# Kernel optimization log

Hardware: AMD Instinct MI355X
Metric: run time of the kernel (lower is better)

## Reference

```python
import jax, jax.numpy as jnp
import numpy as np

LN_EPS = 1e-5


def _mlp(x, W1, b1, W2, b2, g, beta):
    # build_mlp_d: Linear -> ReLU -> Linear -> LayerNorm (mlp_layers=2, lay_norm=True)
    h = jax.nn.relu(x @ W1 + b1)
    h = h @ W2 + b2
    mu = jnp.mean(h, axis=-1, keepdims=True)
    var = jnp.var(h, axis=-1, keepdims=True)
    return (h - mu) * jax.lax.rsqrt(var + LN_EPS) * g + beta


def setup_inputs() -> dict:
    E, N, L, EIF = 524288, 65536, 128, 3
    key = jax.random.key(0)
    ks = iter(jax.random.split(key, 48))
    def rn(shape, s=1.0):
        return jax.random.normal(next(ks), shape, dtype=jnp.float32) * s
    inp = {}
    inp["edge_index"] = jax.random.randint(next(ks), (2, E), 0, N)
    inp["edge_dx_"] = rn((E, 3))
    inp["edge_attr"] = rn((E, EIF))
    for nm in ["vector_a", "vector_b", "vector_c",
               "senders_v_t_", "senders_v_tm1_", "senders_w_t_", "senders_w_tm1_",
               "senders_a_t_", "senders_alpha_t_",
               "receivers_v_t_", "receivers_v_tm1_", "receivers_w_t_", "receivers_w_tm1_",
               "receivers_a_t_", "receivers_alpha_t_"]:
        inp[nm] = rn((E, 3))
    inp["node_latent"] = rn((N, L))
    def mlp_params(pfx, din):
        inp[pfx + "_W1"] = rn((din, L), 0.05)
        inp[pfx + "_b1"] = jnp.zeros((L,), jnp.float32)
        inp[pfx + "_W2"] = rn((L, L), 0.05)
        inp[pfx + "_b2"] = jnp.zeros((L,), jnp.float32)
        inp[pfx + "_g"] = jnp.ones((L,), jnp.float32)
        inp[pfx + "_beta"] = jnp.zeros((L,), jnp.float32)
    mlp_params("fe", 18)        # edge_feat_encoder
    mlp_params("ee", 1 + EIF)   # edge_encoder
    mlp_params("ie", 3 * L)     # interaction_encoder
    return inp


def reference(edge_index, edge_dx_, edge_attr, vector_a, vector_b, vector_c,
              senders_v_t_, senders_v_tm1_, senders_w_t_, senders_w_tm1_,
              senders_a_t_, senders_alpha_t_,
              receivers_v_t_, receivers_v_tm1_, receivers_w_t_, receivers_w_tm1_,
              receivers_a_t_, receivers_alpha_t_,
              node_latent,
              fe_W1, fe_b1, fe_W2, fe_b2, fe_g, fe_beta,
              ee_W1, ee_b1, ee_W2, ee_b2, ee_g, ee_beta,
              ie_W1, ie_b1, ie_W2, ie_b2, ie_g, ie_beta):
    senders, receivers = edge_index[0], edge_index[1]
    basis = jnp.stack([vector_a, vector_b, vector_c], axis=1)  # [E,3,3]
    # Fuse the 12 small bmm projections into two batched einsums.
    s_stack = jnp.stack([senders_v_t_, senders_v_tm1_, senders_w_t_, senders_w_tm1_,
                         senders_a_t_, senders_alpha_t_], axis=1)   # [E,6,3]
    r_stack = jnp.stack([receivers_v_t_, receivers_v_tm1_, receivers_w_t_, receivers_w_tm1_,
                         receivers_a_t_, receivers_alpha_t_], axis=1)
    s_proj = jnp.einsum('eij,ekj->eki', basis, s_stack)  # [E,6,3]
    r_proj = jnp.einsum('eij,ekj->eki', basis, r_stack)
    # signs: -v_t, -v_tm1, -w_t, +w_tm1, -a_t, +alpha_t (receivers side)
    r_sign = jnp.array([-1.0, -1.0, -1.0, 1.0, -1.0, 1.0], jnp.float32)[None, :, None]
    E = s_proj.shape[0]
    senders_features = s_proj.reshape(E, 18)
    receivers_features = (r_proj * r_sign).reshape(E, 18)
    edge_dx_norm = jnp.linalg.norm(edge_dx_, axis=1, keepdims=True)  # [E,1]
    edge_latent = _mlp(jnp.concatenate([edge_dx_norm, edge_attr], axis=1),
                       ee_W1, ee_b1, ee_W2, ee_b2, ee_g, ee_beta)
    senders_latent = _mlp(senders_features, fe_W1, fe_b1, fe_W2, fe_b2, fe_g, fe_beta)
    receivers_latent = _mlp(receivers_features, fe_W1, fe_b1, fe_W2, fe_b2, fe_g, fe_beta)
    node_sum = node_latent[senders] + node_latent[receivers]  # [E,L]
    msg_input = jnp.concatenate([senders_latent + receivers_latent, node_sum, edge_latent], axis=1)
    return _mlp(msg_input, ie_W1, ie_b1, ie_W2, ie_b2, ie_g, ie_beta)
```

## Files before the change

### kernel.cpp

```cpp
#include <hip/hip_runtime.h>

typedef __attribute__((ext_vector_type(4))) float fx4;
typedef __attribute__((ext_vector_type(8))) unsigned short u16x8;
typedef __attribute__((ext_vector_type(8))) __bf16 bf16x8;

static __device__ __forceinline__ unsigned short f2bf(float f) {
  unsigned int u = __builtin_bit_cast(unsigned int, f);
  u += 0x7fffu + ((u >> 16) & 1u);
  return (unsigned short)(u >> 16);
}
static __device__ __forceinline__ fx4 mfma16(u16x8 a, u16x8 b, fx4 c) {
  return __builtin_amdgcn_mfma_f32_16x16x32_bf16(
      __builtin_bit_cast(bf16x8, a), __builtin_bit_cast(bf16x8, b), c, 0, 0, 0);
}

static __device__ __forceinline__ int swz128(int row, int col) {
  return row * 128 + (col ^ ((row & 7) << 3));
}
static __device__ __forceinline__ int swz32(int row, int col) {
  return row * 32 + (col ^ (((row >> 1) & 3) << 3));
}

#define WT_FE1 0
#define WT_FE2 4096
#define WT_EE1 20480
#define WT_EE2 24576
#define WT_A   40960
#define WT_B   57344
#define WT_C   73728
#define WT_IE2 90112
#define WT_TOTAL 106496

__global__ void prep_weights(const float* __restrict__ feW1, const float* __restrict__ feW2,
                             const float* __restrict__ eeW1, const float* __restrict__ eeW2,
                             const float* __restrict__ ieW1, const float* __restrict__ ieW2,
                             unsigned short* __restrict__ wt) {
  int i = blockIdx.x * 256 + threadIdx.x;
  if (i >= WT_TOTAL) return;
  int base, n, k, kpad;
  float val;
  if (i < WT_FE2)      { base = WT_FE1; n = i >> 5; k = i & 31; kpad = 32;
                         val = (k < 18) ? feW1[k * 128 + n] : 0.f; }
  else if (i < WT_EE1) { base = WT_FE2; int j = i - WT_FE2; n = j >> 7; k = j & 127; kpad = 128;
                         val = feW2[k * 128 + n]; }
  else if (i < WT_EE2) { base = WT_EE1; int j = i - WT_EE1; n = j >> 5; k = j & 31; kpad = 32;
                         val = (k < 4) ? eeW1[k * 128 + n] : 0.f; }
  else if (i < WT_A)   { base = WT_EE2; int j = i - WT_EE2; n = j >> 7; k = j & 127; kpad = 128;
                         val = eeW2[k * 128 + n]; }
  else if (i < WT_B)   { base = WT_A;   int j = i - WT_A;   n = j >> 7; k = j & 127; kpad = 128;
                         val = ieW1[k * 128 + n]; }
  else if (i < WT_C)   { base = WT_B;   int j = i - WT_B;   n = j >> 7; k = j & 127; kpad = 128;
                         val = ieW1[(128 + k) * 128 + n]; }
  else if (i < WT_IE2) { base = WT_C;   int j = i - WT_C;   n = j >> 7; k = j & 127; kpad = 128;
                         val = ieW1[(256 + k) * 128 + n]; }
  else                 { base = WT_IE2; int j = i - WT_IE2; n = j >> 7; k = j & 127; kpad = 128;
                         val = ieW2[k * 128 + n]; }
  int dst = (kpad == 32) ? base + n * 32 + (k ^ (((n >> 1) & 3) << 3))
                         : base + n * 128 + (k ^ ((n & 7) << 3));
  wt[dst] = f2bf(val);
}

template<int KPAD, int KT>
static __device__ __forceinline__ void gemm_lds(const unsigned short* As,
                                                const unsigned short* Ws,
                                                fx4* acc, int l16, int lgr) {
#pragma unroll
  for (int kk = 0; kk < KT; kk++) {
    const int k0 = kk * 32 + lgr * 8;
    u16x8 af = *(const u16x8*)(As + ((KPAD == 32) ? swz32(l16, k0) : swz128(l16, k0)));
#pragma unroll
    for (int nt = 0; nt < 8; nt++) {
      const int n = nt * 16 + l16;
      u16x8 bf = *(const u16x8*)(Ws + ((KPAD == 32) ? swz32(n, k0) : swz128(n, k0)));
      acc[nt] = mfma16(af, bf, acc[nt]);
    }
  }
}

static __device__ __forceinline__ void relu_store(fx4* acc, const float* __restrict__ bias,
                                                  unsigned short* dst, int l16, int lgr) {
#pragma unroll
  for (int nt = 0; nt < 8; nt++) {
    const int col = nt * 16 + l16;
    const float b = bias[col];
#pragma unroll
    for (int r = 0; r < 4; r++) {
      float v = acc[nt][r] + b;
      dst[swz128(lgr * 4 + r, col)] = f2bf(v > 0.f ? v : 0.f);
    }
  }
}

static __device__ __forceinline__ void ln_rows(fx4* acc, const float* __restrict__ bias, int l16) {
  float sum[4] = {0, 0, 0, 0}, sq[4] = {0, 0, 0, 0};
#pragma unroll
  for (int nt = 0; nt < 8; nt++) {
    const float b = bias[nt * 16 + l16];
#pragma unroll
    for (int r = 0; r < 4; r++) {
      float v = acc[nt][r] + b; acc[nt][r] = v;
      sum[r] += v; sq[r] += v * v;
    }
  }
#pragma unroll
  for (int r = 0; r < 4; r++) {
    float s_ = sum[r], q_ = sq[r];
#pragma unroll
    for (int m = 1; m < 16; m <<= 1) { s_ += __shfl_xor(s_, m, 64); q_ += __shfl_xor(q_, m, 64); }
    const float mu = s_ * (1.f / 128.f);
    const float rs = rsqrtf(q_ * (1.f / 128.f) - mu * mu + 1e-5f);
#pragma unroll
    for (int nt = 0; nt < 8; nt++) acc[nt][r] = (acc[nt][r] - mu) * rs;
  }
}

struct ParamsFE {
  const float* basis[3];
  const float* sv[6]; const float* rv[6];
  const float* b1; const float* b2; const float* g; const float* be;
};
struct ParamsEE {
  const float* dx; const float* attr;
  const float* b1; const float* b2; const float* g; const float* be;
};

static __device__ __forceinline__ void fe_body(const ParamsFE& p, unsigned short* lds,
                                               const unsigned short* wt, unsigned short* msg,
                                               int bid, int nblocks, int ntiles) {
  const int tid = threadIdx.x;
  const int wave = tid >> 6, lane = tid & 63;
  const int l16 = lane & 15, lgr = lane >> 4;
#pragma unroll
  for (int i = tid * 8; i < 20480; i += 2048)
    *(u16x8*)(lds + i) = *(const u16x8*)(wt + WT_FE1 + i);
  const unsigned short* W1 = lds;
  const unsigned short* W2 = lds + 4096;
  unsigned short* h1 = lds + 20480 + wave * 5120;
  unsigned short* feat = h1 + 4096;
  __syncthreads();
#pragma unroll
  for (int j = 0; j < 4; j++) {
    int c = 18 + lgr * 4 + j;
    if (c < 32) { feat[swz32(l16, c)] = 0; feat[swz32(16 + l16, c)] = 0; }
  }
  const fx4 z4 = {0.f, 0.f, 0.f, 0.f};

  for (int t = bid; t < ntiles; t += nblocks) {
    const int e0 = t * 64 + wave * 16;
    const size_t e = (size_t)(e0 + l16);
    float bx[3][3];
#pragma unroll
    for (int i = 0; i < 3; i++) {
      const float* bp = p.basis[i] + 3 * e;
      bx[i][0] = bp[0]; bx[i][1] = bp[1]; bx[i][2] = bp[2];
    }
#pragma unroll
    for (int k = 0; k < 6; k++) {
      if ((k & 3) == lgr) {
        const float* vs = p.sv[k] + 3 * e;
        const float* vr = p.rv[k] + 3 * e;
        const float s0 = vs[0], s1 = vs[1], s2 = vs[2];
        const float r0 = vr[0], r1 = vr[1], r2 = vr[2];
        const float sgn = (k != 3 && k != 5) ? -1.f : 1.f;
#pragma unroll
        for (int i = 0; i < 3; i++) {
          feat[swz32(l16, k * 3 + i)] =
              f2bf(bx[i][0] * s0 + bx[i][1] * s1 + bx[i][2] * s2);
          feat[swz32(16 + l16, k * 3 + i)] =
              f2bf((bx[i][0] * r0 + bx[i][1] * r1 + bx[i][2] * r2) * sgn);
        }
      }
    }
    fx4 accA[8], accB[8];
#pragma unroll
    for (int b = 0; b < 8; b++) { accA[b] = z4; accB[b] = z4; }
    {
      const int k0 = lgr * 8;
      u16x8 afA = *(const u16x8*)(feat + swz32(l16, k0));
      u16x8 afB = *(const u16x8*)(feat + swz32(16 + l16, k0));
#pragma unroll
      for (int nt = 0; nt < 8; nt++) {
        u16x8 bf = *(const u16x8*)(W1 + swz32(nt * 16 + l16, k0));
        accA[nt] = mfma16(afA, bf, accA[nt]);
        accB[nt] = mfma16(afB, bf, accB[nt]);
      }
    }
    relu_store(accA, p.b1, h1, l16, lgr);
    relu_store(accB, p.b1, h1 + 2048, l16, lgr);
#pragma unroll
    for (int b = 0; b < 8; b++) { accA[b] = z4; accB[b] = z4; }
#pragma unroll
    for (int c = 0; c < 4; c++) {
      const int k0 = c * 32 + lgr * 8;
      u16x8 afA = *(const u16x8*)(h1 + swz128(l16, k0));
      u16x8 afB = *(const u16x8*)(h1 + 2048 + swz128(l16, k0));
#pragma unroll
      for (int nt = 0; nt < 8; nt++) {
        u16x8 bf = *(const u16x8*)(W2 + swz128(nt * 16 + l16, k0));
        accA[nt] = mfma16(afA, bf, accA[nt]);
        accB[nt] = mfma16(afB, bf, accB[nt]);
      }
    }
    ln_rows(accA, p.b2, l16);
    ln_rows(accB, p.b2, l16);
#pragma unroll
    for (int nt = 0; nt < 8; nt++) {
      const int col = nt * 16 + l16;
      const float gg = p.g[col], bb = p.be[col];
#pragma unroll
      for (int r = 0; r < 4; r++)
        msg[(size_t)(e0 + lgr * 4 + r) * 256 + col] =
            f2bf(accA[nt][r] * gg + bb + accB[nt][r] * gg + bb);
    }
  }
}

static __device__ __forceinline__ void ee_body(const ParamsEE& p, unsigned short* lds,
                                               const unsigned short* wt, unsigned short* msg,
                                               int bid, int nblocks, int ntiles) {
  const int tid = threadIdx.x;
  const int wave = tid >> 6, lane = tid & 63;
  const int l16 = lane & 15, lgr = lane >> 4;
#pragma unroll
  for (int i = tid * 8; i < 20480; i += 2048)
    *(u16x8*)(lds + i) = *(const u16x8*)(wt + WT_EE1 + i);
  const unsigned short* W1 = lds;
  const unsigned short* W2 = lds + 4096;
  unsigned short* h1 = lds + 20480 + wave * 2560;
  unsigned short* feat = h1 + 2048;
  __syncthreads();
#pragma unroll
  for (int j = 0; j < 7; j++) feat[swz32(l16, 4 + lgr * 7 + j)] = 0;
  const fx4 z4 = {0.f, 0.f, 0.f, 0.f};

  for (int t = bid; t < ntiles; t += nblocks) {
    const int e0 = t * 64 + wave * 16;
    const size_t e = (size_t)(e0 + l16);
    if (lgr == 0) {
      float d0 = p.dx[3 * e], d1 = p.dx[3 * e + 1], d2 = p.dx[3 * e + 2];
      feat[swz32(l16, 0)] = f2bf(sqrtf(d0 * d0 + d1 * d1 + d2 * d2));
    } else {
      feat[swz32(l16, lgr)] = f2bf(p.attr[3 * e + (lgr - 1)]);
    }
    fx4 acc[8];
#pragma unroll
    for (int b = 0; b < 8; b++) acc[b] = z4;
    gemm_lds<32, 1>(feat, W1, acc, l16, lgr);
    relu_store(acc, p.b1, h1, l16, lgr);
#pragma unroll
    for (int b = 0; b < 8; b++) acc[b] = z4;
    gemm_lds<128, 4>(h1, W2, acc, l16, lgr);
    ln_rows(acc, p.b2, l16);
#pragma unroll
    for (int nt = 0; nt < 8; nt++) {
      const int col = nt * 16 + l16;
      const float gg = p.g[col], bb = p.be[col];
#pragma unroll
      for (int r = 0; r < 4; r++)
        msg[(size_t)(e0 + lgr * 4 + r) * 256 + 128 + col] =
            f2bf(acc[nt][r] * gg + bb);
    }
  }
}

__global__ __launch_bounds__(256) void feee_kernel(ParamsFE pf, ParamsEE pe,
                                                   const unsigned short* wt,
                                                   unsigned short* msg,
                                                   int nfe, int ntiles) {
  extern __shared__ unsigned short lds[];
  if ((int)blockIdx.x < nfe)
    fe_body(pf, lds, wt, msg, blockIdx.x, nfe, ntiles);
  else
    ee_body(pe, lds, wt, msg, blockIdx.x - nfe, gridDim.x - nfe, ntiles);
}

struct ParamsIE {
  const int* eidx;
  const float* nl;
  const float* b1; const float* b2; const float* g; const float* be;
  const unsigned short* wt;
  const unsigned short* msg;
  float* out;
  int E; int ntiles;
};

__global__ __launch_bounds__(512) void ie_kernel(ParamsIE p) {
  extern __shared__ unsigned short dyn[];
  const int tid = threadIdx.x;
  const int wave = tid >> 6, lane = tid & 63;
  const int l16 = lane & 15, lgr = lane >> 4;
#pragma unroll
  for (int i = tid * 8; i < 49152; i += 4096)
    *(u16x8*)(dyn + i) = *(const u16x8*)(p.wt + WT_A + i);
  const unsigned short* WA = dyn;
  const unsigned short* WB = dyn + 16384;
  const unsigned short* WC = dyn + 32768;
  unsigned short* h1 = dyn + 49152 + wave * 2048;
  __syncthreads();
  const fx4 z4 = {0.f, 0.f, 0.f, 0.f};

  for (int t = blockIdx.x; t < p.ntiles; t += gridDim.x) {
    const int e0 = t * 128 + wave * 16;
    const size_t e = (size_t)(e0 + l16);
    const int sidx = p.eidx[e];
    const int ridx = p.eidx[(size_t)p.E + e];
    const unsigned short* mrow = p.msg + e * 256;
    const float* ns = p.nl + (size_t)sidx * 128;
    const float* nr = p.nl + (size_t)ridx * 128;
    u16x8 xs[4], xe[4];
#pragma unroll
    for (int c = 0; c < 4; c++) {
      const int k0 = c * 32 + lgr * 8;
      xs[c] = *(const u16x8*)(mrow + k0);
      xe[c] = *(const u16x8*)(mrow + 128 + k0);
    }
    fx4 acc[8];
#pragma unroll
    for (int b = 0; b < 8; b++) acc[b] = z4;
#pragma unroll
    for (int c = 0; c < 4; c++) {
      const int k0 = c * 32 + lgr * 8;
      fx4 a0 = *(const fx4*)(ns + k0), a1 = *(const fx4*)(ns + k0 + 4);
      fx4 b0 = *(const fx4*)(nr + k0), b1 = *(const fx4*)(nr + k0 + 4);
      u16x8 af;
#pragma unroll
      for (int j = 0; j < 4; j++) { af[j] = f2bf(a0[j] + b0[j]); af[4 + j] = f2bf(a1[j] + b1[j]); }
#pragma unroll
      for (int nt = 0; nt < 8; nt++) {
        u16x8 bf = *(const u16x8*)(WB + swz128(nt * 16 + l16, k0));
        acc[nt] = mfma16(af, bf, acc[nt]);
      }
    }
#pragma unroll
    for (int c = 0; c < 4; c++) {
      const int k0 = c * 32 + lgr * 8;
#pragma unroll
      for (int nt = 0; nt < 8; nt++) {
        u16x8 bf = *(const u16x8*)(WA + swz128(nt * 16 + l16, k0));
        acc[nt] = mfma16(xs[c], bf, acc[nt]);
      }
    }
#pragma unroll
    for (int c = 0; c < 4; c++) {
      const int k0 = c * 32 + lgr * 8;
#pragma unroll
      for (int nt = 0; nt < 8; nt++) {
        u16x8 bf = *(const u16x8*)(WC + swz128(nt * 16 + l16, k0));
        acc[nt] = mfma16(xe[c], bf, acc[nt]);
      }
    }
    relu_store(acc, p.b1, h1, l16, lgr);
#pragma unroll
    for (int b = 0; b < 8; b++) acc[b] = z4;
    gemm_lds<128, 4>(h1, p.wt + WT_IE2, acc, l16, lgr);
    ln_rows(acc, p.b2, l16);
#pragma unroll
    for (int nt = 0; nt < 8; nt++) {
      const int col = nt * 16 + l16;
      const float gg = p.g[col], bb = p.be[col];
#pragma unroll
      for (int r = 0; r < 4; r++)
        p.out[(size_t)(e0 + lgr * 4 + r) * 128 + col] = acc[nt][r] * gg + bb;
    }
  }
}

extern "C" void kernel_launch(void* const* d_in, const int* in_sizes, int n_in,
                              void* d_out, int out_size, void* d_ws, size_t ws_size,
                              hipStream_t stream) {
  (void)n_in; (void)out_size;
  const int E = in_sizes[1] / 3;
  unsigned short* wt = reinterpret_cast<unsigned short*>(d_ws);
  if (ws_size < (size_t)WT_TOTAL * sizeof(unsigned short)) return;

  prep_weights<<<(WT_TOTAL + 255) / 256, 256, 0, stream>>>(
      (const float*)d_in[19], (const float*)d_in[21],
      (const float*)d_in[25], (const float*)d_in[27],
      (const float*)d_in[31], (const float*)d_in[33], wt);

  unsigned short* msg = (unsigned short*)d_out;

  hipFuncSetAttribute((const void*)feee_kernel,
                      hipFuncAttributeMaxDynamicSharedMemorySize, 81920);
  hipFuncSetAttribute((const void*)ie_kernel,
                      hipFuncAttributeMaxDynamicSharedMemorySize, 131072);

  ParamsFE pf;
  for (int i = 0; i < 3; i++) pf.basis[i] = (const float*)d_in[3 + i];
  for (int k = 0; k < 6; k++) { pf.sv[k] = (const float*)d_in[6 + k]; pf.rv[k] = (const float*)d_in[12 + k]; }
  pf.b1 = (const float*)d_in[20]; pf.b2 = (const float*)d_in[22];
  pf.g  = (const float*)d_in[23]; pf.be = (const float*)d_in[24];

  ParamsEE pe;
  pe.dx = (const float*)d_in[1]; pe.attr = (const float*)d_in[2];
  pe.b1 = (const float*)d_in[26]; pe.b2 = (const float*)d_in[28];
  pe.g  = (const float*)d_in[29]; pe.be = (const float*)d_in[30];

  feee_kernel<<<1536, 256, 81920, stream>>>(pf, pe, wt, msg, 1024, E / 64);

  ParamsIE pi;
  pi.eidx = (const int*)d_in[0];
  pi.nl = (const float*)d_in[18];
  pi.b1 = (const float*)d_in[32]; pi.b2 = (const float*)d_in[34];
  pi.g  = (const float*)d_in[35]; pi.be = (const float*)d_in[36];
  pi.wt = wt; pi.msg = msg; pi.out = (float*)d_out;
  pi.E = E; pi.ntiles = E / 128;
  ie_kernel<<<256, 512, 131072, stream>>>(pi);
}
```

Baseline: 523.2 us.

## Software-pipeline edge loads and reorder GEMM chunks to hide gather latency

The interaction-encoder loop now prefetches the next tile's edge indices and message rows while the current tile runs its second GEMM. Within a tile, the node-latent gathers are split into two halves issued ahead of the message-row MFMAs, and the gathered-sum chunk is consumed last. The aim is to hide global and gather latency behind MFMA work. The cost is more live registers, which may lower occupancy or cause spills at 512 threads.

```diff
diff --git a/kernel.cpp b/kernel.cpp
--- a/kernel.cpp
+++ b/kernel.cpp
@@ -298,58 +298,93 @@
   unsigned short* h1 = dyn + 49152 + wave * 2048;
   __syncthreads();
   const fx4 z4 = {0.f, 0.f, 0.f, 0.f};
-
-  for (int t = blockIdx.x; t < p.ntiles; t += gridDim.x) {
+  const int gstride = gridDim.x;
+
+  int t = blockIdx.x;
+  int sidx = 0, ridx = 0;
+  u16x8 xs[4], xe[4];
+  if (t < p.ntiles) {
+    const size_t e = (size_t)(t * 128 + wave * 16 + l16);
+    sidx = p.eidx[e];
+    ridx = p.eidx[(size_t)p.E + e];
+    const unsigned short* mrow = p.msg + e * 256;
+#pragma unroll
+    for (int c = 0; c < 4; c++) {
+      const int k0 = c * 32 + lgr * 8;
+      xs[c] = *(const u16x8*)(mrow + k0);
+      xe[c] = *(const u16x8*)(mrow + 128 + k0);
+    }
+  }
+
+  for (; t < p.ntiles; t += gstride) {
     const int e0 = t * 128 + wave * 16;
-    const size_t e = (size_t)(e0 + l16);
-    const int sidx = p.eidx[e];
-    const int ridx = p.eidx[(size_t)p.E + e];
-    const unsigned short* mrow = p.msg + e * 256;
     const float* ns = p.nl + (size_t)sidx * 128;
     const float* nr = p.nl + (size_t)ridx * 128;
-    u16x8 xs[4], xe[4];
+    fx4 na[2][2], nb[2][2];
+#pragma unroll
+    for (int c = 0; c < 2; c++) {
+      const int k0 = c * 32 + lgr * 8;
+      na[c][0] = *(const fx4*)(ns + k0); na[c][1] = *(const fx4*)(ns + k0 + 4);
+      nb[c][0] = *(const fx4*)(nr + k0); nb[c][1] = *(const fx4*)(nr + k0 + 4);
+    }
+    fx4 acc[8];
+#pragma unroll
+    for (int b = 0; b < 8; b++) acc[b] = z4;
 #pragma unroll
     for (int c = 0; c < 4; c++) {
       const int k0 = c * 32 + lgr * 8;
-      xs[c] = *(const u16x8*)(mrow + k0);
-      xe[c] = *(const u16x8*)(mrow + 128 + k0);
-    }
-    fx4 acc[8];
-#pragma unroll
-    for (int b = 0; b < 8; b++) acc[b] = z4;
+#pragma unroll
+      for (int nt = 0; nt < 8; nt++) {
+        u16x8 bf = *(const u16x8*)(WA + swz128(nt * 16 + l16, k0));
+        acc[nt] = mfma16(xs[c], bf, acc[nt]);
+      }
+    }
+    fx4 nc[2][2], nd[2][2];
+#pragma unroll
+    for (int c = 0; c < 2; c++) {
+      const int k0 = (c + 2) * 32 + lgr * 8;
+      nc[c][0] = *(const fx4*)(ns + k0); nc[c][1] = *(const fx4*)(ns + k0 + 4);
+      nd[c][0] = *(const fx4*)(nr + k0); nd[c][1] = *(const fx4*)(nr + k0 + 4);
+    }
 #pragma unroll
     for (int c = 0; c < 4; c++) {
       const int k0 = c * 32 + lgr * 8;
-      fx4 a0 = *(const fx4*)(ns + k0), a1 = *(const fx4*)(ns + k0 + 4);
-      fx4 b0 = *(const fx4*)(nr + k0), b1 = *(const fx4*)(nr + k0 + 4);
+#pragma unroll
+      for (int nt = 0; nt < 8; nt++) {
+        u16x8 bf = *(const u16x8*)(WC + swz128(nt * 16 + l16, k0));
+        acc[nt] = mfma16(xe[c], bf, acc[nt]);
+      }
+    }
+#pragma unroll
+    for (int c = 0; c < 4; c++) {
+      const int k0 = c * 32 + lgr * 8;
+      fx4 s0 = (c < 2) ? na[c & 1][0] : nc[c & 1][0];
+      fx4 s1 = (c < 2) ? na[c & 1][1] : nc[c & 1][1];
+      fx4 r0 = (c < 2) ? nb[c & 1][0] : nd[c & 1][0];
+      fx4 r1 = (c < 2) ? nb[c & 1][1] : nd[c & 1][1];
       u16x8 af;
 #pragma unroll
-      for (int j = 0; j < 4; j++) { af[j] = f2bf(a0[j] + b0[j]); af[4 + j] = f2bf(a1[j] + b1[j]); }
+      for (int j = 0; j < 4; j++) { af[j] = f2bf(s0[j] + r0[j]); af[4 + j] = f2bf(s1[j] + r1[j]); }
 #pragma unroll
       for (int nt = 0; nt < 8; nt++) {
         u16x8 bf = *(const u16x8*)(WB + swz128(nt * 16 + l16, k0));
         acc[nt] = mfma16(af, bf, acc[nt]);
       }
     }
-#pragma unroll
-    for (int c = 0; c < 4; c++) {
-      const int k0 = c * 32 + lgr * 8;
-#pragma unroll
-      for (int nt = 0; nt < 8; nt++) {
-        u16x8 bf = *(const u16x8*)(WA + swz128(nt * 16 + l16, k0));
-        acc[nt] = mfma16(xs[c], bf, acc[nt]);
-      }
-    }
-#pragma unroll
-    for (int c = 0; c < 4; c++) {
-      const int k0 = c * 32 + lgr * 8;
-#pragma unroll
-      for (int nt = 0; nt < 8; nt++) {
-        u16x8 bf = *(const u16x8*)(WC + swz128(nt * 16 + l16, k0));
-        acc[nt] = mfma16(xe[c], bf, acc[nt]);
-      }
-    }
     relu_store(acc, p.b1, h1, l16, lgr);
+    const int tn = t + gstride;
+    if (tn < p.ntiles) {
+      const size_t en = (size_t)(tn * 128 + wave * 16 + l16);
+      sidx = p.eidx[en];
+      ridx = p.eidx[(size_t)p.E + en];
+      const unsigned short* mrow2 = p.msg + en * 256;
+#pragma unroll
+      for (int c = 0; c < 4; c++) {
+        const int k0 = c * 32 + lgr * 8;
+        xs[c] = *(const u16x8*)(mrow2 + k0);
+        xe[c] = *(const u16x8*)(mrow2 + 128 + k0);
+      }
+    }
 #pragma unroll
     for (int b = 0; b < 8; b++) acc[b] = z4;
     gemm_lds<128, 4>(h1, p.wt + WT_IE2, acc, l16, lgr);
```

After: 518.3 us. No clear change (-0.9%).
